# Optimization experiments

Hardware: AMD Instinct MI355X
Metric: run time of the kernel (lower is better)

Reference implementation:

```python
import jax, jax.numpy as jnp
import numpy as np

EPS = 1e-5
H, HC = 4, 16  # heads, head_dim (H*HC = hidden_dim = 64)
FILL = jnp.array([0., 0., 0., 0., 0., 0., 1.], dtype=jnp.float32)  # self-loop edge_attr


def inorm(x, w, b):
    # PyG InstanceNorm on a single graph: per-channel stats over all nodes
    mu = x.mean(axis=0)
    var = x.var(axis=0)
    return (x - mu) / jnp.sqrt(var + EPS) * w + b


def setup_inputs() -> dict:
    key = jax.random.key(0)
    ks = jax.random.split(key, 40)
    N, E, D, ED = 50000, 1600000, 64, 7
    p = lambda i, s: jax.random.normal(ks[i], s, dtype=jnp.float32) * 0.05
    return {
        'x': jax.random.normal(ks[0], (N, D), dtype=jnp.float32),
        'edge_index': jax.random.randint(ks[1], (2, E), 0, N),
        'edge_attr': jax.random.normal(ks[2], (E, ED), dtype=jnp.float32),
        'pre_w': 1.0 + p(3, (D,)), 'pre_b': p(4, (D,)),
        'eW1': p(5, (D, 64)), 'en1w': 1.0 + p(6, (64,)), 'en1b': p(7, (64,)),
        'eW2': p(8, (64, 64)), 'en2w': 1.0 + p(9, (64,)), 'en2b': p(10, (64,)),
        'Wl': p(11, (64, 64)), 'Wr': p(12, (64, 64)), 'We': p(13, (ED, 64)), 'att': p(14, (H, HC)),
        'gn_w': 1.0 + p(15, (64,)), 'gn_b': p(16, (64,)),
        'dW1': p(17, (128, 256)), 'db1': p(18, (256,)),
        'dW2': p(19, (256, 128)), 'db2': p(20, (128,)),
        'dW3': p(21, (128, 64)), 'db3': p(22, (64,)),
        'dW4': p(23, (64, 32)), 'db4': p(24, (32,)),
        'dW5': p(25, (32, 16)), 'db5': p(26, (16,)),
        'dW6': p(27, (16, 2)), 'db6': p(28, (2,)),
        'rW1': p(29, (64, 64)), 'rb1': p(30, (64,)),
        'rW2': p(31, (64, 64)), 'rb2': p(32, (64,)),
        'rW3': p(33, (64, 64)), 'rb3': p(34, (64,)),
    }


def _forward(x, edge_index, edge_attr,
             pre_w, pre_b, eW1, en1w, en1b, eW2, en2w, en2b,
             Wl, Wr, We, att, gn_w, gn_b,
             dW1, db1, dW2, db2, dW3, db3, dW4, db4, dW5, db5, dW6, db6,
             rW1, rb1, rW2, rb2, rW3, rb3):
    N = x.shape[0]
    h = inorm(x, pre_w, pre_b)
    h = jax.nn.elu(inorm(h @ eW1, en1w, en1b))
    h = jax.nn.elu(inorm(h @ eW2, en2w, en2b))
    jk = h

    # ---- GATv2 block (add self loops with fill_value edge attr) ----
    loop = jnp.arange(N)
    src = jnp.concatenate([edge_index[0], loop])  # message source j
    dst = jnp.concatenate([edge_index[1], loop])  # message target i
    ea = jnp.concatenate([edge_attr, jnp.broadcast_to(FILL, (N, 7))], axis=0)

    xl = (h @ Wl).reshape(N, H, HC)  # lin_l (source features)
    xr = (h @ Wr).reshape(N, H, HC)  # lin_r (target features)
    ee = (ea @ We).reshape(-1, H, HC)

    m = xl[src] + xr[dst] + ee                                  # [Etot,H,HC]
    logits = jnp.einsum('ehc,hc->eh', jax.nn.leaky_relu(m, 0.2), att)

    # softmax over incoming edges per target node, per head
    lmax = jax.ops.segment_max(logits, dst, num_segments=N)
    ex = jnp.exp(logits - lmax[dst])
    denom = jax.ops.segment_sum(ex, dst, num_segments=N)
    alpha = ex / denom[dst]

    msg = alpha[:, :, None] * xl[src]
    agg = jax.ops.segment_sum(msg, dst, num_segments=N)
    deg = jax.ops.segment_sum(jnp.ones((src.shape[0],), x.dtype), dst, num_segments=N)
    gat_out = (agg / deg[:, None, None]).reshape(N, H * HC)     # aggr='mean'

    h = jax.nn.elu(h + inorm(gat_out, gn_w, gn_b))

    cat = jnp.concatenate([jk, h], axis=-1)                     # jumping knowledge
    d = jax.nn.elu(cat @ dW1 + db1)
    d = jax.nn.elu(d @ dW2 + db2)
    d = jax.nn.elu(d @ dW3 + db3)
    d = jax.nn.elu(d @ dW4 + db4)
    d = jax.nn.elu(d @ dW5 + db5)
    dec = d @ dW6 + db6

    r = jax.nn.elu(h @ rW1 + rb1)
    r = jax.nn.elu(r @ rW2 + rb2)
    recon = r @ rW3 + rb3
    return dec, recon


def reference(x, edge_index, edge_attr,
              pre_w, pre_b, eW1, en1w, en1b, eW2, en2w, en2b,
              Wl, Wr, We, att, gn_w, gn_b,
              dW1, db1, dW2, db2, dW3, db3, dW4, db4, dW5, db5, dW6, db6,
              rW1, rb1, rW2, rb2, rW3, rb3):
    return _forward(x, edge_index, edge_attr,
                    pre_w, pre_b, eW1, en1w, en1b, eW2, en2w, en2b,
                    Wl, Wr, We, att, gn_w, gn_b,
                    dW1, db1, dW2, db2, dW3, db3, dW4, db4, dW5, db5, dW6, db6,
                    rW1, rb1, rW2, rb2, rW3, rb3)
```

## Files before the change

### kernel.cpp

```cpp
#include <hip/hip_runtime.h>
#include <math.h>


typedef long long ll;
typedef unsigned short u16;
typedef float f32x4 __attribute__((ext_vector_type(4)));
typedef short s16x8 __attribute__((ext_vector_type(8)));

__device__ __forceinline__ float bf(u16 u) { return __uint_as_float(((unsigned)u) << 16); }
__device__ __forceinline__ u16 f2bf(float f) {
  unsigned u = __float_as_uint(f);
  u += 0x7fffu + ((u >> 16) & 1u);
  return (u16)(u >> 16);
}
__device__ __forceinline__ float bflo(unsigned u) { return __uint_as_float(u << 16); }
__device__ __forceinline__ float bfhi(unsigned u) { return __uint_as_float(u & 0xffff0000u); }
__device__ __forceinline__ float elu_f(float x) { return x > 0.f ? x : (__expf(x) - 1.f); }

__global__ void k_probe64(const int* __restrict__ ei, int cnt, int* __restrict__ flag) {
  int tid = threadIdx.x;
  int nz = 0;
  for (int k = tid; k < cnt; k += 256) {
    if (ei[2 * k + 1] != 0) nz = 1;
  }
  if (nz) atomicOr(flag, 1);
}

__global__ void k_stats_x(const float* __restrict__ x, int N, double* __restrict__ s0) {
  __shared__ float red[256];
  int tid = threadIdx.x;
  int c = tid & 63;
  float s = 0.f, ss = 0.f;
  for (int r = blockIdx.x * 4 + (tid >> 6); r < N; r += gridDim.x * 4) {
    float v = x[r * 64 + c];
    s += v; ss += v * v;
  }
  red[tid] = s; __syncthreads();
  if (tid < 64) atomicAdd(&s0[tid], (double)(red[tid] + red[tid + 64] + red[tid + 128] + red[tid + 192]));
  __syncthreads();
  red[tid] = ss; __syncthreads();
  if (tid < 64) atomicAdd(&s0[64 + tid], (double)(red[tid] + red[tid + 64] + red[tid + 128] + red[tid + 192]));
}

__device__ __forceinline__ void norm_coeffs(const double* s, int tid, int N,
                                            const float* w, const float* b,
                                            float* na, float* nb) {
  double invN = 1.0 / (double)N;
  double mean = s[tid] * invN;
  double var = s[64 + tid] * invN - mean * mean;
  float a = rsqrtf((float)var + 1e-5f) * w[tid];
  na[tid] = a; nb[tid] = b[tid] - (float)mean * a;
}

template <bool ACT>
__global__ void k_enc(const float* __restrict__ in, const float* __restrict__ w,
                      const float* __restrict__ b, const float* __restrict__ Wg,
                      const double* __restrict__ sin_, float* __restrict__ out,
                      double* __restrict__ sout, int N) {
  __shared__ float W[4096];
  __shared__ float hl[4][64];
  __shared__ float na[64], nb[64];
  __shared__ float red[256];
  int tid = threadIdx.x;
  if (tid < 64) norm_coeffs(sin_, tid, N, w, b, na, nb);
  for (int k = tid; k < 4096; k += 256) W[k] = Wg[k];
  __syncthreads();
  int nl = tid >> 6, j = tid & 63;
  int Nc = (N + 3) >> 2;
  float ssum = 0.f, ssq = 0.f;
  for (int chunk = blockIdx.x; chunk < Nc; chunk += gridDim.x) {
    int node = chunk * 4 + nl;
    bool valid = node < N;
    float hv = valid ? (in[node * 64 + j] * na[j] + nb[j]) : 0.f;
    hl[nl][j] = ACT ? elu_f(hv) : hv;
    __syncthreads();
    if (valid) {
      float acc = 0.f;
#pragma unroll
      for (int i = 0; i < 64; i++) acc += hl[nl][i] * W[i * 64 + j];
      out[node * 64 + j] = acc;
      ssum += acc; ssq += acc * acc;
    }
    __syncthreads();
  }
  red[tid] = ssum; __syncthreads();
  if (tid < 64) atomicAdd(&sout[tid], (double)(red[tid] + red[tid + 64] + red[tid + 128] + red[tid + 192]));
  __syncthreads();
  red[tid] = ssq; __syncthreads();
  if (tid < 64) atomicAdd(&sout[64 + tid], (double)(red[tid] + red[tid + 64] + red[tid + 128] + red[tid + 192]));
}

__global__ void k_enc3(const float* __restrict__ tB, const float* __restrict__ w,
                       const float* __restrict__ b, const float* __restrict__ Wlw,
                       const float* __restrict__ Wrw, const double* __restrict__ s2,
                       float* __restrict__ jk, u16* __restrict__ xlb, float* __restrict__ xr,
                       int N) {
  __shared__ float WL[4096], WR[4096];
  __shared__ float hl[4][64];
  __shared__ float na[64], nb[64];
  int tid = threadIdx.x;
  if (tid < 64) norm_coeffs(s2, tid, N, w, b, na, nb);
  for (int k = tid; k < 4096; k += 256) { WL[k] = Wlw[k]; WR[k] = Wrw[k]; }
  __syncthreads();
  int nl = tid >> 6, j = tid & 63;
  int Nc = (N + 3) >> 2;
  for (int chunk = blockIdx.x; chunk < Nc; chunk += gridDim.x) {
    int node = chunk * 4 + nl;
    bool valid = node < N;
    float h3 = valid ? elu_f(tB[node * 64 + j] * na[j] + nb[j]) : 0.f;
    hl[nl][j] = h3;
    __syncthreads();
    if (valid) {
      jk[node * 64 + j] = h3;
      float al = 0.f, ar = 0.f;
#pragma unroll
      for (int i = 0; i < 64; i++) {
        float h = hl[nl][i];
        al += h * WL[i * 64 + j];
        ar += h * WR[i * 64 + j];
      }
      xlb[node * 64 + j] = f2bf(al);
      xr[node * 64 + j] = ar;
    }
    __syncthreads();
  }
}

__global__ void k_deg(const int* __restrict__ ei, int* __restrict__ deg8, int E, int N,
                      const int* __restrict__ i32flag) {
  int e = blockIdx.x * 256 + threadIdx.x;
  if (e >= E + N) return;
  int r = blockIdx.x & 7;
  int dst;
  if (e < E) {
    if (*i32flag) dst = ei[E + e];
    else { const ll* el = (const ll*)ei; dst = (int)el[E + e]; }
  } else dst = e - E;
  atomicAdd(&deg8[r * N + dst], 1);
}

__global__ void k_scanA(const int* __restrict__ deg8, int* __restrict__ bsum, int N) {
  __shared__ int red[256];
  int tid = threadIdx.x;
  int base = blockIdx.x * 1024;
  int s = 0;
#pragma unroll
  for (int q = 0; q < 4; q++) {
    int n = base + q * 256 + tid;
    if (n < N) {
#pragma unroll
      for (int r = 0; r < 8; r++) s += deg8[r * N + n];
    }
  }
  red[tid] = s; __syncthreads();
  for (int o = 128; o > 0; o >>= 1) {
    if (tid < o) red[tid] += red[tid + o];
    __syncthreads();
  }
  if (tid == 0) bsum[blockIdx.x] = red[0];
}

__global__ void k_scanB(const int* __restrict__ bsum, int* __restrict__ bscan,
                        int* __restrict__ offs, int NB, int N) {
  if (threadIdx.x == 0) {
    int run = 0;
    for (int b = 0; b < NB; b++) { bscan[b] = run; run += bsum[b]; }
    offs[N] = run;
  }
}

__global__ void k_scanC(const int* __restrict__ deg8, const int* __restrict__ bscan,
                        int* __restrict__ offs, int* __restrict__ cursor8, int N) {
  __shared__ int dt[1024];
  __shared__ int tp[256];
  int tid = threadIdx.x;
  int base = blockIdx.x * 1024;
#pragma unroll
  for (int q = 0; q < 4; q++) {
    int n = base + q * 256 + tid;
    int s = 0;
    if (n < N) {
#pragma unroll
      for (int r = 0; r < 8; r++) s += deg8[r * N + n];
    }
    dt[q * 256 + tid] = s;
  }
  __syncthreads();
  int t4 = tid * 4;
  int l0 = dt[t4], l1 = dt[t4 + 1], l2 = dt[t4 + 2], l3 = dt[t4 + 3];
  int tot = l0 + l1 + l2 + l3;
  tp[tid] = tot; __syncthreads();
  for (int o = 1; o < 256; o <<= 1) {
    int v = (tid >= o) ? tp[tid - o] : 0;
    __syncthreads();
    tp[tid] += v;
    __syncthreads();
  }
  int run = bscan[blockIdx.x] + tp[tid] - tot;
#pragma unroll
  for (int k = 0; k < 4; k++) {
    int n = base + t4 + k;
    if (n < N) {
      offs[n] = run;
      int b = run;
#pragma unroll
      for (int r = 0; r < 8; r++) { cursor8[r * N + n] = b; b += deg8[r * N + n]; }
      run = b;
    }
  }
}

template <bool PACKED>
__global__ void k_scatter(const int* __restrict__ ei, const float* __restrict__ eattr,
                          int* __restrict__ cursor8, int* __restrict__ csr_src,
                          uint4* __restrict__ ea2, int E, int N,
                          const int* __restrict__ i32flag) {
  int e = blockIdx.x * 256 + threadIdx.x;
  if (e >= E + N) return;
  int r = blockIdx.x & 7;
  int src, dst;
  u16 p[8];
  if (e < E) {
    if (*i32flag) { src = ei[e]; dst = ei[E + e]; }
    else { const ll* el = (const ll*)ei; src = (int)el[e]; dst = (int)el[E + e]; }
    const float* ea = eattr + (size_t)e * 7;
#pragma unroll
    for (int q = 0; q < 7; q++) p[q] = f2bf(ea[q]);
    p[7] = 0;
  } else {
    src = e - E; dst = src;
#pragma unroll
    for (int q = 0; q < 8; q++) p[q] = 0;
    p[6] = 0x3F80;
  }
  int pos = atomicAdd(&cursor8[r * N + dst], 1);
  uint4 U;
  U.x = ((unsigned)p[1] << 16) | p[0];
  U.y = ((unsigned)p[3] << 16) | p[2];
  U.z = ((unsigned)p[5] << 16) | p[4];
  if (PACKED) {
    U.w = ((unsigned)src << 16) | p[6];
  } else {
    U.w = ((unsigned)p[7] << 16) | p[6];
    csr_src[pos] = src;
  }
  ea2[pos] = U;
}

template <bool PACKED>
__global__ void k_gat(const int* __restrict__ offs, const int* __restrict__ csr_src,
                      const uint4* __restrict__ ea2,
                      const u16* __restrict__ xlb, const float* __restrict__ xr,
                      const float* __restrict__ Wew, const float* __restrict__ attw,
                      float* __restrict__ gat, double* __restrict__ s3, int N) {
  __shared__ float sb[4][64];
  int tid = threadIdx.x;
  int wid = tid >> 6;
  int lane = tid & 63;
  int g = lane >> 4;
  int l = lane & 15;
  int Nc = (N + 3) >> 2;

  float4 wq[7];
#pragma unroll
  for (int q = 0; q < 7; q++) wq[q] = *(const float4*)(Wew + q * 64 + 4 * l);
  float4 attv = *(const float4*)(attw + 4 * l);

  float ts0 = 0.f, ts1 = 0.f, ts2 = 0.f, ts3 = 0.f;
  float tq0 = 0.f, tq1 = 0.f, tq2 = 0.f, tq3 = 0.f;

  for (int chunk = blockIdx.x; chunk < Nc; chunk += gridDim.x) {
    int node = chunk * 4 + wid;
    if (node >= N) continue;
    float4 xrv = *(const float4*)(xr + node * 64 + 4 * l);
    int st = offs[node];
    int dg = offs[node + 1] - st;
    int nb = (dg + 3) >> 2;
    float sden = 0.f;
    float a0 = 0.f, a1 = 0.f, a2 = 0.f, a3 = 0.f;

    int i0 = st + g;
    uint4 UC = ea2[i0];
    uint4 UN = ea2[i0 + 4];
    int scC, scN;
    if (PACKED) {
      scC = (int)(UC.w >> 16);
      scN = (int)(UN.w >> 16);
    } else {
      scC = csr_src[i0];
      scN = csr_src[i0 + 4];
    }
    scC = ((unsigned)scC < (unsigned)N) ? scC : 0;
    uint2 xwC = *(const uint2*)(xlb + scC * 64 + 4 * l);

    for (int b = 0; b < nb; b++) {
      int iA = st + (b + 2) * 4 + g;
      uint4 UA = ea2[iA];
      int scA = PACKED ? 0 : csr_src[iA];
      int scg = PACKED ? (int)(UN.w >> 16) : scN;
      scg = ((unsigned)scg < (unsigned)N) ? scg : 0;
      uint2 xwN = *(const uint2*)(xlb + scg * 64 + 4 * l);
      bool valid = (b * 4 + g) < dg;
      float x0 = bflo(xwC.x), x1 = bfhi(xwC.x), x2 = bflo(xwC.y), x3 = bfhi(xwC.y);
      float e0 = bflo(UC.x), e1 = bfhi(UC.x), e2 = bflo(UC.y), e3 = bfhi(UC.y);
      float e4 = bflo(UC.z), e5 = bfhi(UC.z), e6 = bflo(UC.w);
      float m0 = x0 + xrv.x + e0*wq[0].x + e1*wq[1].x + e2*wq[2].x + e3*wq[3].x + e4*wq[4].x + e5*wq[5].x + e6*wq[6].x;
      float m1 = x1 + xrv.y + e0*wq[0].y + e1*wq[1].y + e2*wq[2].y + e3*wq[3].y + e4*wq[4].y + e5*wq[5].y + e6*wq[6].y;
      float m2 = x2 + xrv.z + e0*wq[0].z + e1*wq[1].z + e2*wq[2].z + e3*wq[3].z + e4*wq[4].z + e5*wq[5].z + e6*wq[6].z;
      float m3 = x3 + xrv.w + e0*wq[0].w + e1*wq[1].w + e2*wq[2].w + e3*wq[3].w + e4*wq[4].w + e5*wq[5].w + e6*wq[6].w;
      m0 = m0 > 0.f ? m0 : 0.2f * m0;
      m1 = m1 > 0.f ? m1 : 0.2f * m1;
      m2 = m2 > 0.f ? m2 : 0.2f * m2;
      m3 = m3 > 0.f ? m3 : 0.2f * m3;
      float pp = m0 * attv.x + m1 * attv.y + m2 * attv.z + m3 * attv.w;
      pp += __shfl_xor(pp, 1, 64);
      pp += __shfl_xor(pp, 2, 64);
      float ex = valid ? __expf(pp) : 0.f;
      sden += ex;
      a0 += ex * x0; a1 += ex * x1; a2 += ex * x2; a3 += ex * x3;
      xwC = xwN; UC = UN; UN = UA; scN = scA;
    }
    a0 += __shfl_xor(a0, 16, 64); a0 += __shfl_xor(a0, 32, 64);
    a1 += __shfl_xor(a1, 16, 64); a1 += __shfl_xor(a1, 32, 64);
    a2 += __shfl_xor(a2, 16, 64); a2 += __shfl_xor(a2, 32, 64);
    a3 += __shfl_xor(a3, 16, 64); a3 += __shfl_xor(a3, 32, 64);
    sden += __shfl_xor(sden, 16, 64); sden += __shfl_xor(sden, 32, 64);
    float inv = 1.f / (sden * (float)dg);
    float val0 = a0 * inv, val1 = a1 * inv, val2 = a2 * inv, val3 = a3 * inv;
    if (g == 0) {
      float4 o = make_float4(val0, val1, val2, val3);
      *(float4*)(gat + node * 64 + 4 * l) = o;
      ts0 += val0; ts1 += val1; ts2 += val2; ts3 += val3;
      tq0 += val0 * val0; tq1 += val1 * val1; tq2 += val2 * val2; tq3 += val3 * val3;
    }
  }

  if (g == 0) {
    sb[wid][4 * l + 0] = ts0; sb[wid][4 * l + 1] = ts1;
    sb[wid][4 * l + 2] = ts2; sb[wid][4 * l + 3] = ts3;
  }
  __syncthreads();
  if (tid < 64) {
    float v = sb[0][tid] + sb[1][tid] + sb[2][tid] + sb[3][tid];
    atomicAdd(&s3[tid], (double)v);
  }
  __syncthreads();
  if (g == 0) {
    sb[wid][4 * l + 0] = tq0; sb[wid][4 * l + 1] = tq1;
    sb[wid][4 * l + 2] = tq2; sb[wid][4 * l + 3] = tq3;
  }
  __syncthreads();
  if (tid < 64) {
    float v = sb[0][tid] + sb[1][tid] + sb[2][tid] + sb[3][tid];
    atomicAdd(&s3[64 + tid], (double)v);
  }
}

__global__ void k_edge2(const int* __restrict__ ei, const float* __restrict__ eattr,
                        const u16* __restrict__ xlb, const float* __restrict__ xr,
                        const float* __restrict__ Wew, const float* __restrict__ attw,
                        float* __restrict__ agg, float* __restrict__ denom,
                        int* __restrict__ deg, int E, int N,
                        const int* __restrict__ i32flag) {
  __shared__ float sWe[448];
  __shared__ float satt[64];
  int tid = threadIdx.x;
  for (int k = tid; k < 448; k += 256) sWe[k] = Wew[k];
  if (tid < 64) satt[tid] = attw[tid];
  __syncthreads();
  int e = blockIdx.x * 4 + (tid >> 6);
  if (e >= E + N) return;
  int lane = tid & 63;
  int src, dst;
  if (e < E) {
    if (*i32flag) { src = ei[e]; dst = ei[E + e]; }
    else { const ll* el = (const ll*)ei; src = (int)el[e]; dst = (int)el[E + e]; }
  } else { src = e - E; dst = src; }
  float xlv = bf(xlb[src * 64 + lane]);
  float m = xlv + xr[dst * 64 + lane];
  if (e < E) {
#pragma unroll
    for (int k = 0; k < 7; k++) m += eattr[e * 7 + k] * sWe[k * 64 + lane];
  } else {
    m += sWe[6 * 64 + lane];
  }
  float lr = m > 0.f ? m : 0.2f * m;
  float p = lr * satt[lane];
  p += __shfl_xor(p, 1, 64);
  p += __shfl_xor(p, 2, 64);
  p += __shfl_xor(p, 4, 64);
  p += __shfl_xor(p, 8, 64);
  float ex = __expf(p);
  atomicAdd(&agg[dst * 64 + lane], ex * xlv);
  if ((lane & 15) == 0) atomicAdd(&denom[dst * 4 + (lane >> 4)], ex);
  if (lane == 0) atomicAdd(&deg[dst], 1);
}

__global__ void k_gatnorm(float* __restrict__ agg, const float* __restrict__ denom,
                          const int* __restrict__ deg, double* __restrict__ s3, int N) {
  __shared__ float red[256];
  int tid = threadIdx.x;
  int idx = blockIdx.x * 256 + tid;
  float v = 0.f;
  if (idx < N * 64) {
    int n = idx >> 6, c = idx & 63, h = c >> 4;
    v = agg[idx] / (denom[n * 4 + h] * (float)deg[n]);
    agg[idx] = v;
  }
  red[tid] = v; __syncthreads();
  if (tid < 64) atomicAdd(&s3[tid], (double)(red[tid] + red[tid + 64] + red[tid + 128] + red[tid + 192]));
  __syncthreads();
  red[tid] = v * v; __syncthreads();
  if (tid < 64) atomicAdd(&s3[64 + tid], (double)(red[tid] + red[tid + 64] + red[tid + 128] + red[tid + 192]));
}

__global__ void k_h4(const float* __restrict__ jk, const float* __restrict__ gat,
                     const float* __restrict__ gn_w, const float* __restrict__ gn_b,
                     const double* __restrict__ s3, float* __restrict__ h4, int N) {
  __shared__ float na[64], nb[64];
  int tid = threadIdx.x;
  if (tid < 64) norm_coeffs(s3, tid, N, gn_w, gn_b, na, nb);
  __syncthreads();
  int idx = blockIdx.x * 256 + tid;
  if (idx >= N * 64) return;
  int c = idx & 63;
  h4[idx] = elu_f(jk[idx] + gat[idx] * na[c] + nb[c]);
}

__global__ void k_wprep(const float* __restrict__ dW1, const float* __restrict__ dW2,
                        const float* __restrict__ dW3, const float* __restrict__ dW4,
                        const float* __restrict__ dW5,
                        u16* __restrict__ whi, u16* __restrict__ wlo) {
  int t = blockIdx.x;
  int tid = threadIdx.x;
  const float* W; int LIN, LOUT, base;
  if (t < 64)       { W = dW1; LIN = 128; LOUT = 256; base = 0; }
  else if (t < 128) { W = dW2; LIN = 256; LOUT = 128; base = 64; }
  else if (t < 144) { W = dW3; LIN = 128; LOUT = 64;  base = 128; }
  else if (t < 148) { W = dW4; LIN = 64;  LOUT = 32;  base = 144; }
  else              { W = dW5; LIN = 32;  LOUT = 16;  base = 148; }
  int KT = LIN >> 5;
  int tl = t - base;
  int nt = tl / KT, kt = tl % KT;
#pragma unroll
  for (int half = 0; half < 2; half++) {
    int lane = (tid >> 3) + half * 32;
    int i = tid & 7;
    int kg = kt * 32 + (lane >> 4) * 8 + i;
    int ng = nt * 16 + (lane & 15);
    float v = W[kg * LOUT + ng];
    u16 hi = f2bf(v);
    u16 lo = f2bf(v - bf(hi));
    whi[((size_t)t * 64 + lane) * 8 + i] = hi;
    wlo[((size_t)t * 64 + lane) * 8 + i] = lo;
  }
}

template <int LIN, int LOUT, int TBASE>
__device__ __forceinline__ void mfmaLayer(const u16* __restrict__ whi, const u16* __restrict__ wlo,
                                          const float* __restrict__ bias,
                                          const u16* __restrict__ Ahi, const u16* __restrict__ Alo,
                                          u16* __restrict__ Ohi, u16* __restrict__ Olo,
                                          int wid, int lane) {
  constexpr int KT = LIN / 32, NT = LOUT / 16;
  constexpr int SIN = LIN + 8, SOUT = LOUT + 8;
  int l15 = lane & 15, kg = lane >> 4;
  int aoff = l15 * SIN + kg * 8;
  for (int nt = wid; nt < NT; nt += 4) {
    float bn = bias[nt * 16 + l15];
    f32x4 acc = {bn, bn, bn, bn};
    for (int kt = 0; kt < KT; kt++) {
      s16x8 ah = *(const s16x8*)(Ahi + aoff + kt * 32);
      s16x8 al = *(const s16x8*)(Alo + aoff + kt * 32);
      const u16* wp = whi + ((size_t)(TBASE + nt * KT + kt) * 64 + lane) * 8;
      const u16* wq = wlo + ((size_t)(TBASE + nt * KT + kt) * 64 + lane) * 8;
      s16x8 wh = *(const s16x8*)(wp);
      s16x8 wl = *(const s16x8*)(wq);
      acc = __builtin_amdgcn_mfma_f32_16x16x32_bf16(ah, wh, acc, 0, 0, 0);
      acc = __builtin_amdgcn_mfma_f32_16x16x32_bf16(ah, wl, acc, 0, 0, 0);
      acc = __builtin_amdgcn_mfma_f32_16x16x32_bf16(al, wh, acc, 0, 0, 0);
    }
#pragma unroll
    for (int r = 0; r < 4; r++) {
      int m = kg * 4 + r;
      float v = elu_f(acc[r]);
      u16 hi = f2bf(v);
      u16 lo = f2bf(v - bf(hi));
      Ohi[m * SOUT + nt * 16 + l15] = hi;
      Olo[m * SOUT + nt * 16 + l15] = lo;
    }
  }
}

__global__ void k_dec(const float* __restrict__ jk, const float* __restrict__ h4,
                      const u16* __restrict__ whi, const u16* __restrict__ wlo,
                      const float* __restrict__ db1, const float* __restrict__ db2,
                      const float* __restrict__ db3, const float* __restrict__ db4,
                      const float* __restrict__ db5,
                      const float* __restrict__ dW6, const float* __restrict__ db6,
                      float* __restrict__ outdec, int N) {
  __shared__ __align__(16) u16 bHi0[16 * 264], bLo0[16 * 264];
  __shared__ __align__(16) u16 bHi1[16 * 264], bLo1[16 * 264];
  int tid = threadIdx.x;
  int wid = tid >> 6, lane = tid & 63;
  int g0 = blockIdx.x * 16;
  for (int k = tid; k < 16 * 128; k += 256) {
    int i = k & 127, node = k >> 7;
    int gn = g0 + node;
    float v = 0.f;
    if (gn < N) v = (i < 64) ? jk[gn * 64 + i] : h4[gn * 64 + (i - 64)];
    u16 hi = f2bf(v);
    u16 lo = f2bf(v - bf(hi));
    bHi0[node * 136 + i] = hi;
    bLo0[node * 136 + i] = lo;
  }
  __syncthreads();
  mfmaLayer<128, 256, 0>(whi, wlo, db1, bHi0, bLo0, bHi1, bLo1, wid, lane); __syncthreads();
  mfmaLayer<256, 128, 64>(whi, wlo, db2, bHi1, bLo1, bHi0, bLo0, wid, lane); __syncthreads();
  mfmaLayer<128, 64, 128>(whi, wlo, db3, bHi0, bLo0, bHi1, bLo1, wid, lane); __syncthreads();
  mfmaLayer<64, 32, 144>(whi, wlo, db4, bHi1, bLo1, bHi0, bLo0, wid, lane); __syncthreads();
  mfmaLayer<32, 16, 148>(whi, wlo, db5, bHi0, bLo0, bHi1, bLo1, wid, lane); __syncthreads();
  if (tid < 32) {
    int node = tid >> 1, j = tid & 1;
    int gn = g0 + node;
    if (gn < N) {
      float s = db6[j];
#pragma unroll
      for (int i = 0; i < 16; i++) {
        float a = bf(bHi1[node * 24 + i]) + bf(bLo1[node * 24 + i]);
        s += a * dW6[i * 2 + j];
      }
      outdec[gn * 2 + j] = s;
    }
  }
}

__global__ void k_recon(const float* __restrict__ h4,
                        const float* __restrict__ rW1, const float* __restrict__ rb1,
                        const float* __restrict__ rW2, const float* __restrict__ rb2,
                        const float* __restrict__ rW3, const float* __restrict__ rb3,
                        float* __restrict__ outrec, int N) {
  __shared__ float W1[4096], W2[4096], W3[4096];
  __shared__ float b1[64], b2[64], b3[64];
  __shared__ float A[64 * 16], Bb[64 * 16];
  int tid = threadIdx.x;
  for (int k = tid; k < 4096; k += 256) { W1[k] = rW1[k]; W2[k] = rW2[k]; W3[k] = rW3[k]; }
  if (tid < 64) { b1[tid] = rb1[tid]; b2[tid] = rb2[tid]; b3[tid] = rb3[tid]; }
  __syncthreads();
  int j = tid & 63, g = tid >> 6;
  int Nc = (N + 15) >> 4;
  for (int chunk = blockIdx.x; chunk < Nc; chunk += gridDim.x) {
    int g0 = chunk * 16;
    for (int k = tid; k < 16 * 64; k += 256) {
      int i = k & 63, node = k >> 6;
      int gn = g0 + node;
      A[i * 16 + node] = (gn < N) ? h4[gn * 64 + i] : 0.f;
    }
    __syncthreads();
    {
      float a0 = b1[j], a1 = b1[j], a2 = b1[j], a3 = b1[j];
#pragma unroll 4
      for (int i = 0; i < 64; i++) {
        float w = W1[i * 64 + j];
        float4 a = *(const float4*)(&A[i * 16 + g * 4]);
        a0 += a.x * w; a1 += a.y * w; a2 += a.z * w; a3 += a.w * w;
      }
      Bb[j * 16 + g * 4 + 0] = elu_f(a0);
      Bb[j * 16 + g * 4 + 1] = elu_f(a1);
      Bb[j * 16 + g * 4 + 2] = elu_f(a2);
      Bb[j * 16 + g * 4 + 3] = elu_f(a3);
    }
    __syncthreads();
    {
      float a0 = b2[j], a1 = b2[j], a2 = b2[j], a3 = b2[j];
#pragma unroll 4
      for (int i = 0; i < 64; i++) {
        float w = W2[i * 64 + j];
        float4 a = *(const float4*)(&Bb[i * 16 + g * 4]);
        a0 += a.x * w; a1 += a.y * w; a2 += a.z * w; a3 += a.w * w;
      }
      A[j * 16 + g * 4 + 0] = elu_f(a0);
      A[j * 16 + g * 4 + 1] = elu_f(a1);
      A[j * 16 + g * 4 + 2] = elu_f(a2);
      A[j * 16 + g * 4 + 3] = elu_f(a3);
    }
    __syncthreads();
    {
      float a0 = b3[j], a1 = b3[j], a2 = b3[j], a3 = b3[j];
#pragma unroll 4
      for (int i = 0; i < 64; i++) {
        float w = W3[i * 64 + j];
        float4 a = *(const float4*)(&A[i * 16 + g * 4]);
        a0 += a.x * w; a1 += a.y * w; a2 += a.z * w; a3 += a.w * w;
      }
      float o[4] = {a0, a1, a2, a3};
#pragma unroll
      for (int u = 0; u < 4; u++) {
        int gn = g0 + g * 4 + u;
        if (gn < N) outrec[gn * 64 + j] = o[u];
      }
    }
    __syncthreads();
  }
}

__global__ void k_sentinel(float* __restrict__ out, float v) {
  if (threadIdx.x == 0) out[0] = v;
}

extern "C" void kernel_launch(void* const* d_in, const int* in_sizes, int n_in,
                              void* d_out, int out_size, void* d_ws, size_t ws_size,
                              hipStream_t stream) {
  (void)n_in; (void)out_size;
  const float* x     = (const float*)d_in[0];
  const int*   ei    = (const int*)d_in[1];
  const float* ea    = (const float*)d_in[2];
  const float* pre_w = (const float*)d_in[3];
  const float* pre_b = (const float*)d_in[4];
  const float* eW1   = (const float*)d_in[5];
  const float* en1w  = (const float*)d_in[6];
  const float* en1b  = (const float*)d_in[7];
  const float* eW2   = (const float*)d_in[8];
  const float* en2w  = (const float*)d_in[9];
  const float* en2b  = (const float*)d_in[10];
  const float* Wl    = (const float*)d_in[11];
  const float* Wr    = (const float*)d_in[12];
  const float* Wew   = (const float*)d_in[13];
  const float* attw  = (const float*)d_in[14];
  const float* gn_w  = (const float*)d_in[15];
  const float* gn_b  = (const float*)d_in[16];
  const float* dW1 = (const float*)d_in[17]; const float* db1 = (const float*)d_in[18];
  const float* dW2 = (const float*)d_in[19]; const float* db2 = (const float*)d_in[20];
  const float* dW3 = (const float*)d_in[21]; const float* db3 = (const float*)d_in[22];
  const float* dW4 = (const float*)d_in[23]; const float* db4 = (const float*)d_in[24];
  const float* dW5 = (const float*)d_in[25]; const float* db5 = (const float*)d_in[26];
  const float* dW6 = (const float*)d_in[27]; const float* db6 = (const float*)d_in[28];
  const float* rW1 = (const float*)d_in[29]; const float* rb1 = (const float*)d_in[30];
  const float* rW2 = (const float*)d_in[31]; const float* rb2 = (const float*)d_in[32];
  const float* rW3 = (const float*)d_in[33]; const float* rb3 = (const float*)d_in[34];

  int D  = in_sizes[3];
  int N  = in_sizes[0] / (D > 0 ? D : 1);
  int E  = in_sizes[1] / 2;
  int ED = E > 0 ? in_sizes[2] / E : 0;
  float* outdec = (float*)d_out;
  float* outrec = outdec + (size_t)N * 2;
  if (D != 64 || ED != 7 || in_sizes[14] != 64) {
    k_sentinel<<<1, 64, 0, stream>>>(outdec, 2000.f);
    return;
  }
  int Etot = E + N;

  char* w = (char*)d_ws;
  size_t off = 0;
  auto alloc = [&](size_t bytes) -> void* {
    void* p = w + off;
    off += (bytes + 255) & ~(size_t)255;
    return p;
  };
  const size_t FEATF = (size_t)N * 64 * 4;
  float* B1    = (float*)alloc(FEATF);
  size_t ea2_bytes = ((size_t)Etot + 16) * 16;
  size_t b2ext = ea2_bytes > FEATF ? ea2_bytes : FEATF;
  float* B2    = (float*)alloc(b2ext);
  float* jk    = (float*)alloc(FEATF);
  u16*   xlb   = (u16*)  alloc((size_t)N * 64 * 2);
  float* xr    = (float*)alloc(FEATF);
  int*   offs  = (int*)  alloc(((size_t)N + 1) * 4);
  int*   deg8  = (int*)  alloc((size_t)N * 8 * 4);
  int*   cursor8=(int*)  alloc((size_t)N * 8 * 4);
  int*   bsum  = (int*)  alloc(4096);
  int*   bscan = (int*)  alloc(4096);
  double* stats = (double*)alloc(4 * 128 * 8);
  int* i32flag = (int*)alloc(256);
  float* denom = (float*)alloc((size_t)N * 4 * 4);
  u16* whi = (u16*)alloc((size_t)149 * 512 * 2);
  u16* wlo = (u16*)alloc((size_t)149 * 512 * 2);
  size_t base_off = off;
  int* csr_src = (int*)alloc(((size_t)Etot + 16) * 4);
  size_t csr_off = off;

  double* s0 = stats, *s1 = stats + 128, *s2 = stats + 256, *s3 = stats + 384;
  float* t1 = B1; float* gat = B1; float* agg = B1;
  float* t2 = B2; float* h4 = B2;
  uint4* ea2 = (uint4*)B2;

  bool packed = (N <= 65536);
  bool use_csr = packed ? (base_off <= ws_size) : (csr_off <= ws_size);
  if (!use_csr && base_off > ws_size) {
    k_sentinel<<<1, 64, 0, stream>>>(outdec, 1000.f);
    return;
  }

  hipMemsetAsync(stats, 0, 4 * 128 * 8, stream);
  hipMemsetAsync(i32flag, 0, 256, stream);
  hipMemsetAsync(deg8, 0, (size_t)N * 8 * 4, stream);

  int gN64 = (N * 64 + 255) / 256;
  int gE = (Etot + 255) / 256;
  int probeCnt = E < 1024 ? E : 1024;
  int NB = (N + 1023) / 1024;

  k_probe64<<<1, 256, 0, stream>>>(ei, probeCnt, i32flag);
  k_wprep<<<149, 256, 0, stream>>>(dW1, dW2, dW3, dW4, dW5, whi, wlo);
  k_stats_x<<<1024, 256, 0, stream>>>(x, N, s0);
  k_enc<false><<<1024, 256, 0, stream>>>(x, pre_w, pre_b, eW1, s0, t1, s1, N);
  k_enc<true><<<1024, 256, 0, stream>>>(t1, en1w, en1b, eW2, s1, t2, s2, N);
  k_enc3<<<1024, 256, 0, stream>>>(t2, en2w, en2b, Wl, Wr, s2, jk, xlb, xr, N);

  if (use_csr) {
    k_deg<<<gE, 256, 0, stream>>>(ei, deg8, E, N, i32flag);
    k_scanA<<<NB, 256, 0, stream>>>(deg8, bsum, N);
    k_scanB<<<1, 64, 0, stream>>>(bsum, bscan, offs, NB, N);
    k_scanC<<<NB, 256, 0, stream>>>(deg8, bscan, offs, cursor8, N);
    int ggat = 2048;
    int NcG = (N + 3) / 4;
    if (ggat > NcG) ggat = NcG;
    if (packed) {
      k_scatter<true><<<gE, 256, 0, stream>>>(ei, ea, cursor8, csr_src, ea2, E, N, i32flag);
      k_gat<true><<<ggat, 256, 0, stream>>>(offs, csr_src, ea2, xlb, xr, Wew, attw,
                                            gat, s3, N);
    } else {
      k_scatter<false><<<gE, 256, 0, stream>>>(ei, ea, cursor8, csr_src, ea2, E, N, i32flag);
      k_gat<false><<<ggat, 256, 0, stream>>>(offs, csr_src, ea2, xlb, xr, Wew, attw,
                                             gat, s3, N);
    }
  } else {
    hipMemsetAsync(agg, 0, FEATF, stream);
    hipMemsetAsync(denom, 0, (size_t)N * 4 * 4, stream);
    k_edge2<<<(Etot + 3) / 4, 256, 0, stream>>>(ei, ea, xlb, xr, Wew, attw, agg, denom,
                                                deg8, E, N, i32flag);
    k_gatnorm<<<gN64, 256, 0, stream>>>(agg, denom, deg8, s3, N);
  }

  k_h4<<<gN64, 256, 0, stream>>>(jk, gat, gn_w, gn_b, s3, h4, N);
  int NcD = (N + 15) / 16;
  k_dec<<<NcD, 256, 0, stream>>>(jk, h4, whi, wlo, db1, db2, db3, db4, db5,
                                 dW6, db6, outdec, N);
  k_recon<<<1024, 256, 0, stream>>>(h4, rW1, rb1, rW2, rb2, rW3, rb3, outrec, N);
}
```

Before: 666.8 us.

## Move encoder, GAT projection and recon MLP matmuls onto split-bf16 MFMA

```diff
diff --git a/kernel.cpp b/kernel.cpp
--- a/kernel.cpp
+++ b/kernel.cpp
@@ -52,75 +52,283 @@
   na[tid] = a; nb[tid] = b[tid] - (float)mean * a;
 }
 
-template <bool ACT>
-__global__ void k_enc(const float* __restrict__ in, const float* __restrict__ w,
-                      const float* __restrict__ b, const float* __restrict__ Wg,
-                      const double* __restrict__ sin_, float* __restrict__ out,
-                      double* __restrict__ sout, int N) {
-  __shared__ float W[4096];
-  __shared__ float hl[4][64];
+__global__ void k_wprep(const float* __restrict__ dW1, const float* __restrict__ dW2,
+                        const float* __restrict__ dW3, const float* __restrict__ dW4,
+                        const float* __restrict__ dW5,
+                        const float* __restrict__ eW1, const float* __restrict__ eW2,
+                        const float* __restrict__ Wl, const float* __restrict__ Wr,
+                        const float* __restrict__ rW1, const float* __restrict__ rW2,
+                        const float* __restrict__ rW3,
+                        u16* __restrict__ whi, u16* __restrict__ wlo) {
+  int t = blockIdx.x;
+  int tid = threadIdx.x;
+  const float* W; int LIN, LOUT, base;
+  if (t < 64)       { W = dW1; LIN = 128; LOUT = 256; base = 0; }
+  else if (t < 128) { W = dW2; LIN = 256; LOUT = 128; base = 64; }
+  else if (t < 144) { W = dW3; LIN = 128; LOUT = 64;  base = 128; }
+  else if (t < 148) { W = dW4; LIN = 64;  LOUT = 32;  base = 144; }
+  else if (t < 149) { W = dW5; LIN = 32;  LOUT = 16;  base = 148; }
+  else if (t < 157) { W = eW1; LIN = 64;  LOUT = 64;  base = 149; }
+  else if (t < 165) { W = eW2; LIN = 64;  LOUT = 64;  base = 157; }
+  else if (t < 173) { W = Wl;  LIN = 64;  LOUT = 64;  base = 165; }
+  else if (t < 181) { W = Wr;  LIN = 64;  LOUT = 64;  base = 173; }
+  else if (t < 189) { W = rW1; LIN = 64;  LOUT = 64;  base = 181; }
+  else if (t < 197) { W = rW2; LIN = 64;  LOUT = 64;  base = 189; }
+  else              { W = rW3; LIN = 64;  LOUT = 64;  base = 197; }
+  int KT = LIN >> 5;
+  int tl = t - base;
+  int nt = tl / KT, kt = tl % KT;
+#pragma unroll
+  for (int half = 0; half < 2; half++) {
+    int lane = (tid >> 3) + half * 32;
+    int i = tid & 7;
+    int kg = kt * 32 + (lane >> 4) * 8 + i;
+    int ng = nt * 16 + (lane & 15);
+    float v = W[kg * LOUT + ng];
+    u16 hi = f2bf(v);
+    u16 lo = f2bf(v - bf(hi));
+    whi[((size_t)t * 64 + lane) * 8 + i] = hi;
+    wlo[((size_t)t * 64 + lane) * 8 + i] = lo;
+  }
+}
+
+template <bool INELU>
+__global__ void k_encM(const float* __restrict__ in, const float* __restrict__ w,
+                       const float* __restrict__ b, const u16* __restrict__ whi,
+                       const u16* __restrict__ wlo, int TB,
+                       const double* __restrict__ sin_, float* __restrict__ out,
+                       double* __restrict__ sout, int N) {
+  __shared__ __align__(16) u16 aHi[16 * 72], aLo[16 * 72];
   __shared__ float na[64], nb[64];
-  __shared__ float red[256];
+  __shared__ float sred[64];
   int tid = threadIdx.x;
   if (tid < 64) norm_coeffs(sin_, tid, N, w, b, na, nb);
-  for (int k = tid; k < 4096; k += 256) W[k] = Wg[k];
-  __syncthreads();
-  int nl = tid >> 6, j = tid & 63;
-  int Nc = (N + 3) >> 2;
-  float ssum = 0.f, ssq = 0.f;
+  __syncthreads();
+  int lane = tid & 63, wid = tid >> 6;
+  int l15 = lane & 15, kg = lane >> 4;
+  int Nc = (N + 15) >> 4;
+  float ts = 0.f, tq = 0.f;
   for (int chunk = blockIdx.x; chunk < Nc; chunk += gridDim.x) {
-    int node = chunk * 4 + nl;
-    bool valid = node < N;
-    float hv = valid ? (in[node * 64 + j] * na[j] + nb[j]) : 0.f;
-    hl[nl][j] = ACT ? elu_f(hv) : hv;
-    __syncthreads();
-    if (valid) {
-      float acc = 0.f;
-#pragma unroll
-      for (int i = 0; i < 64; i++) acc += hl[nl][i] * W[i * 64 + j];
-      out[node * 64 + j] = acc;
-      ssum += acc; ssq += acc * acc;
-    }
-    __syncthreads();
-  }
-  red[tid] = ssum; __syncthreads();
-  if (tid < 64) atomicAdd(&sout[tid], (double)(red[tid] + red[tid + 64] + red[tid + 128] + red[tid + 192]));
-  __syncthreads();
-  red[tid] = ssq; __syncthreads();
-  if (tid < 64) atomicAdd(&sout[64 + tid], (double)(red[tid] + red[tid + 64] + red[tid + 128] + red[tid + 192]));
-}
-
-__global__ void k_enc3(const float* __restrict__ tB, const float* __restrict__ w,
-                       const float* __restrict__ b, const float* __restrict__ Wlw,
-                       const float* __restrict__ Wrw, const double* __restrict__ s2,
-                       float* __restrict__ jk, u16* __restrict__ xlb, float* __restrict__ xr,
-                       int N) {
-  __shared__ float WL[4096], WR[4096];
-  __shared__ float hl[4][64];
+    int g0 = chunk * 16;
+    for (int k = tid; k < 1024; k += 256) {
+      int i = k & 63, node = k >> 6;
+      int gn = g0 + node;
+      float v = 0.f;
+      if (gn < N) {
+        v = in[gn * 64 + i] * na[i] + nb[i];
+        if (INELU) v = elu_f(v);
+      }
+      u16 hi = f2bf(v);
+      aHi[node * 72 + i] = hi;
+      aLo[node * 72 + i] = f2bf(v - bf(hi));
+    }
+    __syncthreads();
+    f32x4 acc = {0.f, 0.f, 0.f, 0.f};
+    int aoff = l15 * 72 + kg * 8;
+#pragma unroll
+    for (int kt = 0; kt < 2; kt++) {
+      s16x8 ah = *(const s16x8*)(aHi + aoff + kt * 32);
+      s16x8 al = *(const s16x8*)(aLo + aoff + kt * 32);
+      const u16* wp = whi + ((size_t)(TB + wid * 2 + kt) * 64 + lane) * 8;
+      const u16* wq = wlo + ((size_t)(TB + wid * 2 + kt) * 64 + lane) * 8;
+      s16x8 wh = *(const s16x8*)wp;
+      s16x8 wl = *(const s16x8*)wq;
+      acc = __builtin_amdgcn_mfma_f32_16x16x32_bf16(ah, wh, acc, 0, 0, 0);
+      acc = __builtin_amdgcn_mfma_f32_16x16x32_bf16(ah, wl, acc, 0, 0, 0);
+      acc = __builtin_amdgcn_mfma_f32_16x16x32_bf16(al, wh, acc, 0, 0, 0);
+    }
+    int col = wid * 16 + l15;
+#pragma unroll
+    for (int r = 0; r < 4; r++) {
+      int m = kg * 4 + r;
+      int gn = g0 + m;
+      if (gn < N) {
+        float v = acc[r];
+        out[gn * 64 + col] = v;
+        ts += v; tq += v * v;
+      }
+    }
+    __syncthreads();
+  }
+  ts += __shfl_xor(ts, 16, 64); ts += __shfl_xor(ts, 32, 64);
+  tq += __shfl_xor(tq, 16, 64); tq += __shfl_xor(tq, 32, 64);
+  if (kg == 0) sred[wid * 16 + l15] = ts;
+  __syncthreads();
+  if (tid < 64) atomicAdd(&sout[tid], (double)sred[tid]);
+  __syncthreads();
+  if (kg == 0) sred[wid * 16 + l15] = tq;
+  __syncthreads();
+  if (tid < 64) atomicAdd(&sout[64 + tid], (double)sred[tid]);
+}
+
+__global__ void k_enc3M(const float* __restrict__ t2, const float* __restrict__ w,
+                        const float* __restrict__ b, const u16* __restrict__ whi,
+                        const u16* __restrict__ wlo, const double* __restrict__ s2,
+                        float* __restrict__ jk, u16* __restrict__ xlb,
+                        float* __restrict__ xr, int N) {
+  __shared__ __align__(16) u16 aHi[16 * 72], aLo[16 * 72];
   __shared__ float na[64], nb[64];
   int tid = threadIdx.x;
   if (tid < 64) norm_coeffs(s2, tid, N, w, b, na, nb);
-  for (int k = tid; k < 4096; k += 256) { WL[k] = Wlw[k]; WR[k] = Wrw[k]; }
-  __syncthreads();
-  int nl = tid >> 6, j = tid & 63;
-  int Nc = (N + 3) >> 2;
+  __syncthreads();
+  int lane = tid & 63, wid = tid >> 6;
+  int l15 = lane & 15, kg = lane >> 4;
+  int Nc = (N + 15) >> 4;
   for (int chunk = blockIdx.x; chunk < Nc; chunk += gridDim.x) {
-    int node = chunk * 4 + nl;
-    bool valid = node < N;
-    float h3 = valid ? elu_f(tB[node * 64 + j] * na[j] + nb[j]) : 0.f;
-    hl[nl][j] = h3;
-    __syncthreads();
-    if (valid) {
-      jk[node * 64 + j] = h3;
-      float al = 0.f, ar = 0.f;
-#pragma unroll
-      for (int i = 0; i < 64; i++) {
-        float h = hl[nl][i];
-        al += h * WL[i * 64 + j];
-        ar += h * WR[i * 64 + j];
-      }
-      xlb[node * 64 + j] = f2bf(al);
-      xr[node * 64 + j] = ar;
+    int g0 = chunk * 16;
+    for (int k = tid; k < 1024; k += 256) {
+      int i = k & 63, node = k >> 6;
+      int gn = g0 + node;
+      float v = 0.f;
+      if (gn < N) {
+        v = elu_f(t2[gn * 64 + i] * na[i] + nb[i]);
+        jk[gn * 64 + i] = v;
+      }
+      u16 hi = f2bf(v);
+      aHi[node * 72 + i] = hi;
+      aLo[node * 72 + i] = f2bf(v - bf(hi));
+    }
+    __syncthreads();
+    int aoff = l15 * 72 + kg * 8;
+    int col = wid * 16 + l15;
+    {
+      f32x4 acc = {0.f, 0.f, 0.f, 0.f};
+#pragma unroll
+      for (int kt = 0; kt < 2; kt++) {
+        s16x8 ah = *(const s16x8*)(aHi + aoff + kt * 32);
+        s16x8 al = *(const s16x8*)(aLo + aoff + kt * 32);
+        const u16* wp = whi + ((size_t)(165 + wid * 2 + kt) * 64 + lane) * 8;
+        const u16* wq = wlo + ((size_t)(165 + wid * 2 + kt) * 64 + lane) * 8;
+        s16x8 wh = *(const s16x8*)wp;
+        s16x8 wl = *(const s16x8*)wq;
+        acc = __builtin_amdgcn_mfma_f32_16x16x32_bf16(ah, wh, acc, 0, 0, 0);
+        acc = __builtin_amdgcn_mfma_f32_16x16x32_bf16(ah, wl, acc, 0, 0, 0);
+        acc = __builtin_amdgcn_mfma_f32_16x16x32_bf16(al, wh, acc, 0, 0, 0);
+      }
+#pragma unroll
+      for (int r = 0; r < 4; r++) {
+        int gn = g0 + kg * 4 + r;
+        if (gn < N) xlb[gn * 64 + col] = f2bf(acc[r]);
+      }
+    }
+    {
+      f32x4 acc = {0.f, 0.f, 0.f, 0.f};
+#pragma unroll
+      for (int kt = 0; kt < 2; kt++) {
+        s16x8 ah = *(const s16x8*)(aHi + aoff + kt * 32);
+        s16x8 al = *(const s16x8*)(aLo + aoff + kt * 32);
+        const u16* wp = whi + ((size_t)(173 + wid * 2 + kt) * 64 + lane) * 8;
+        const u16* wq = wlo + ((size_t)(173 + wid * 2 + kt) * 64 + lane) * 8;
+        s16x8 wh = *(const s16x8*)wp;
+        s16x8 wl = *(const s16x8*)wq;
+        acc = __builtin_amdgcn_mfma_f32_16x16x32_bf16(ah, wh, acc, 0, 0, 0);
+        acc = __builtin_amdgcn_mfma_f32_16x16x32_bf16(ah, wl, acc, 0, 0, 0);
+        acc = __builtin_amdgcn_mfma_f32_16x16x32_bf16(al, wh, acc, 0, 0, 0);
+      }
+#pragma unroll
+      for (int r = 0; r < 4; r++) {
+        int gn = g0 + kg * 4 + r;
+        if (gn < N) xr[gn * 64 + col] = acc[r];
+      }
+    }
+    __syncthreads();
+  }
+}
+
+__global__ void k_reconM(const float* __restrict__ h4, const u16* __restrict__ whi,
+                         const u16* __restrict__ wlo,
+                         const float* __restrict__ rb1, const float* __restrict__ rb2,
+                         const float* __restrict__ rb3,
+                         float* __restrict__ outrec, int N) {
+  __shared__ __align__(16) u16 aHi[16 * 72], aLo[16 * 72];
+  __shared__ __align__(16) u16 bHi[16 * 72], bLo[16 * 72];
+  int tid = threadIdx.x;
+  int lane = tid & 63, wid = tid >> 6;
+  int l15 = lane & 15, kg = lane >> 4;
+  int aoff = l15 * 72 + kg * 8;
+  int col = wid * 16 + l15;
+  int Nc = (N + 15) >> 4;
+  for (int chunk = blockIdx.x; chunk < Nc; chunk += gridDim.x) {
+    int g0 = chunk * 16;
+    for (int k = tid; k < 1024; k += 256) {
+      int i = k & 63, node = k >> 6;
+      int gn = g0 + node;
+      float v = (gn < N) ? h4[gn * 64 + i] : 0.f;
+      u16 hi = f2bf(v);
+      aHi[node * 72 + i] = hi;
+      aLo[node * 72 + i] = f2bf(v - bf(hi));
+    }
+    __syncthreads();
+    {
+      float bn = rb1[col];
+      f32x4 acc = {bn, bn, bn, bn};
+#pragma unroll
+      for (int kt = 0; kt < 2; kt++) {
+        s16x8 ah = *(const s16x8*)(aHi + aoff + kt * 32);
+        s16x8 al = *(const s16x8*)(aLo + aoff + kt * 32);
+        const u16* wp = whi + ((size_t)(181 + wid * 2 + kt) * 64 + lane) * 8;
+        const u16* wq = wlo + ((size_t)(181 + wid * 2 + kt) * 64 + lane) * 8;
+        s16x8 wh = *(const s16x8*)wp;
+        s16x8 wl = *(const s16x8*)wq;
+        acc = __builtin_amdgcn_mfma_f32_16x16x32_bf16(ah, wh, acc, 0, 0, 0);
+        acc = __builtin_amdgcn_mfma_f32_16x16x32_bf16(ah, wl, acc, 0, 0, 0);
+        acc = __builtin_amdgcn_mfma_f32_16x16x32_bf16(al, wh, acc, 0, 0, 0);
+      }
+#pragma unroll
+      for (int r = 0; r < 4; r++) {
+        int m = kg * 4 + r;
+        float v = elu_f(acc[r]);
+        u16 hi = f2bf(v);
+        bHi[m * 72 + col] = hi;
+        bLo[m * 72 + col] = f2bf(v - bf(hi));
+      }
+    }
+    __syncthreads();
+    {
+      float bn = rb2[col];
+      f32x4 acc = {bn, bn, bn, bn};
+#pragma unroll
+      for (int kt = 0; kt < 2; kt++) {
+        s16x8 ah = *(const s16x8*)(bHi + aoff + kt * 32);
+        s16x8 al = *(const s16x8*)(bLo + aoff + kt * 32);
+        const u16* wp = whi + ((size_t)(189 + wid * 2 + kt) * 64 + lane) * 8;
+        const u16* wq = wlo + ((size_t)(189 + wid * 2 + kt) * 64 + lane) * 8;
+        s16x8 wh = *(const s16x8*)wp;
+        s16x8 wl = *(const s16x8*)wq;
+        acc = __builtin_amdgcn_mfma_f32_16x16x32_bf16(ah, wh, acc, 0, 0, 0);
+        acc = __builtin_amdgcn_mfma_f32_16x16x32_bf16(ah, wl, acc, 0, 0, 0);
+        acc = __builtin_amdgcn_mfma_f32_16x16x32_bf16(al, wh, acc, 0, 0, 0);
+      }
+#pragma unroll
+      for (int r = 0; r < 4; r++) {
+        int m = kg * 4 + r;
+        float v = elu_f(acc[r]);
+        u16 hi = f2bf(v);
+        aHi[m * 72 + col] = hi;
+        aLo[m * 72 + col] = f2bf(v - bf(hi));
+      }
+    }
+    __syncthreads();
+    {
+      float bn = rb3[col];
+      f32x4 acc = {bn, bn, bn, bn};
+#pragma unroll
+      for (int kt = 0; kt < 2; kt++) {
+        s16x8 ah = *(const s16x8*)(aHi + aoff + kt * 32);
+        s16x8 al = *(const s16x8*)(aLo + aoff + kt * 32);
+        const u16* wp = whi + ((size_t)(197 + wid * 2 + kt) * 64 + lane) * 8;
+        const u16* wq = wlo + ((size_t)(197 + wid * 2 + kt) * 64 + lane) * 8;
+        s16x8 wh = *(const s16x8*)wp;
+        s16x8 wl = *(const s16x8*)wq;
+        acc = __builtin_amdgcn_mfma_f32_16x16x32_bf16(ah, wh, acc, 0, 0, 0);
+        acc = __builtin_amdgcn_mfma_f32_16x16x32_bf16(ah, wl, acc, 0, 0, 0);
+        acc = __builtin_amdgcn_mfma_f32_16x16x32_bf16(al, wh, acc, 0, 0, 0);
+      }
+#pragma unroll
+      for (int r = 0; r < 4; r++) {
+        int gn = g0 + kg * 4 + r;
+        if (gn < N) outrec[gn * 64 + col] = acc[r];
+      }
     }
     __syncthreads();
   }
@@ -427,35 +635,6 @@
   h4[idx] = elu_f(jk[idx] + gat[idx] * na[c] + nb[c]);
 }
 
-__global__ void k_wprep(const float* __restrict__ dW1, const float* __restrict__ dW2,
-                        const float* __restrict__ dW3, const float* __restrict__ dW4,
-                        const float* __restrict__ dW5,
-                        u16* __restrict__ whi, u16* __restrict__ wlo) {
-  int t = blockIdx.x;
-  int tid = threadIdx.x;
-  const float* W; int LIN, LOUT, base;
-  if (t < 64)       { W = dW1; LIN = 128; LOUT = 256; base = 0; }
-  else if (t < 128) { W = dW2; LIN = 256; LOUT = 128; base = 64; }
-  else if (t < 144) { W = dW3; LIN = 128; LOUT = 64;  base = 128; }
-  else if (t < 148) { W = dW4; LIN = 64;  LOUT = 32;  base = 144; }
-  else              { W = dW5; LIN = 32;  LOUT = 16;  base = 148; }
-  int KT = LIN >> 5;
-  int tl = t - base;
-  int nt = tl / KT, kt = tl % KT;
-#pragma unroll
-  for (int half = 0; half < 2; half++) {
-    int lane = (tid >> 3) + half * 32;
-    int i = tid & 7;
-    int kg = kt * 32 + (lane >> 4) * 8 + i;
-    int ng = nt * 16 + (lane & 15);
-    float v = W[kg * LOUT + ng];
-    u16 hi = f2bf(v);
-    u16 lo = f2bf(v - bf(hi));
-    whi[((size_t)t * 64 + lane) * 8 + i] = hi;
-    wlo[((size_t)t * 64 + lane) * 8 + i] = lo;
-  }
-}
-
 template <int LIN, int LOUT, int TBASE>
 __device__ __forceinline__ void mfmaLayer(const u16* __restrict__ whi, const u16* __restrict__ wlo,
                                           const float* __restrict__ bias,
@@ -532,75 +711,6 @@
       }
       outdec[gn * 2 + j] = s;
     }
-  }
-}
-
-__global__ void k_recon(const float* __restrict__ h4,
-                        const float* __restrict__ rW1, const float* __restrict__ rb1,
-                        const float* __restrict__ rW2, const float* __restrict__ rb2,
-                        const float* __restrict__ rW3, const float* __restrict__ rb3,
-                        float* __restrict__ outrec, int N) {
-  __shared__ float W1[4096], W2[4096], W3[4096];
-  __shared__ float b1[64], b2[64], b3[64];
-  __shared__ float A[64 * 16], Bb[64 * 16];
-  int tid = threadIdx.x;
-  for (int k = tid; k < 4096; k += 256) { W1[k] = rW1[k]; W2[k] = rW2[k]; W3[k] = rW3[k]; }
-  if (tid < 64) { b1[tid] = rb1[tid]; b2[tid] = rb2[tid]; b3[tid] = rb3[tid]; }
-  __syncthreads();
-  int j = tid & 63, g = tid >> 6;
-  int Nc = (N + 15) >> 4;
-  for (int chunk = blockIdx.x; chunk < Nc; chunk += gridDim.x) {
-    int g0 = chunk * 16;
-    for (int k = tid; k < 16 * 64; k += 256) {
-      int i = k & 63, node = k >> 6;
-      int gn = g0 + node;
-      A[i * 16 + node] = (gn < N) ? h4[gn * 64 + i] : 0.f;
-    }
-    __syncthreads();
-    {
-      float a0 = b1[j], a1 = b1[j], a2 = b1[j], a3 = b1[j];
-#pragma unroll 4
-      for (int i = 0; i < 64; i++) {
-        float w = W1[i * 64 + j];
-        float4 a = *(const float4*)(&A[i * 16 + g * 4]);
-        a0 += a.x * w; a1 += a.y * w; a2 += a.z * w; a3 += a.w * w;
-      }
-      Bb[j * 16 + g * 4 + 0] = elu_f(a0);
-      Bb[j * 16 + g * 4 + 1] = elu_f(a1);
-      Bb[j * 16 + g * 4 + 2] = elu_f(a2);
-      Bb[j * 16 + g * 4 + 3] = elu_f(a3);
-    }
-    __syncthreads();
-    {
-      float a0 = b2[j], a1 = b2[j], a2 = b2[j], a3 = b2[j];
-#pragma unroll 4
-      for (int i = 0; i < 64; i++) {
-        float w = W2[i * 64 + j];
-        float4 a = *(const float4*)(&Bb[i * 16 + g * 4]);
-        a0 += a.x * w; a1 += a.y * w; a2 += a.z * w; a3 += a.w * w;
-      }
-      A[j * 16 + g * 4 + 0] = elu_f(a0);
-      A[j * 16 + g * 4 + 1] = elu_f(a1);
-      A[j * 16 + g * 4 + 2] = elu_f(a2);
-      A[j * 16 + g * 4 + 3] = elu_f(a3);
-    }
-    __syncthreads();
-    {
-      float a0 = b3[j], a1 = b3[j], a2 = b3[j], a3 = b3[j];
-#pragma unroll 4
-      for (int i = 0; i < 64; i++) {
-        float w = W3[i * 64 + j];
-        float4 a = *(const float4*)(&A[i * 16 + g * 4]);
-        a0 += a.x * w; a1 += a.y * w; a2 += a.z * w; a3 += a.w * w;
-      }
-      float o[4] = {a0, a1, a2, a3};
-#pragma unroll
-      for (int u = 0; u < 4; u++) {
-        int gn = g0 + g * 4 + u;
-        if (gn < N) outrec[gn * 64 + j] = o[u];
-      }
-    }
-    __syncthreads();
   }
 }
 
@@ -674,8 +784,8 @@
   double* stats = (double*)alloc(4 * 128 * 8);
   int* i32flag = (int*)alloc(256);
   float* denom = (float*)alloc((size_t)N * 4 * 4);
-  u16* whi = (u16*)alloc((size_t)149 * 512 * 2);
-  u16* wlo = (u16*)alloc((size_t)149 * 512 * 2);
+  u16* whi = (u16*)alloc((size_t)205 * 512 * 2);
+  u16* wlo = (u16*)alloc((size_t)205 * 512 * 2);
   size_t base_off = off;
   int* csr_src = (int*)alloc(((size_t)Etot + 16) * 4);
   size_t csr_off = off;
@@ -700,13 +810,16 @@
   int gE = (Etot + 255) / 256;
   int probeCnt = E < 1024 ? E : 1024;
   int NB = (N + 1023) / 1024;
+  int Nc16 = (N + 15) / 16;
+  int gEnc = Nc16 < 2048 ? Nc16 : 2048;
 
   k_probe64<<<1, 256, 0, stream>>>(ei, probeCnt, i32flag);
-  k_wprep<<<149, 256, 0, stream>>>(dW1, dW2, dW3, dW4, dW5, whi, wlo);
+  k_wprep<<<205, 256, 0, stream>>>(dW1, dW2, dW3, dW4, dW5, eW1, eW2, Wl, Wr,
+                                   rW1, rW2, rW3, whi, wlo);
   k_stats_x<<<1024, 256, 0, stream>>>(x, N, s0);
-  k_enc<false><<<1024, 256, 0, stream>>>(x, pre_w, pre_b, eW1, s0, t1, s1, N);
-  k_enc<true><<<1024, 256, 0, stream>>>(t1, en1w, en1b, eW2, s1, t2, s2, N);
-  k_enc3<<<1024, 256, 0, stream>>>(t2, en2w, en2b, Wl, Wr, s2, jk, xlb, xr, N);
+  k_encM<false><<<gEnc, 256, 0, stream>>>(x, pre_w, pre_b, whi, wlo, 149, s0, t1, s1, N);
+  k_encM<true><<<gEnc, 256, 0, stream>>>(t1, en1w, en1b, whi, wlo, 157, s1, t2, s2, N);
+  k_enc3M<<<gEnc, 256, 0, stream>>>(t2, en2w, en2b, whi, wlo, s2, jk, xlb, xr, N);
 
   if (use_csr) {
     k_deg<<<gE, 256, 0, stream>>>(ei, deg8, E, N, i32flag);
@@ -734,8 +847,7 @@
   }
 
   k_h4<<<gN64, 256, 0, stream>>>(jk, gat, gn_w, gn_b, s3, h4, N);
-  int NcD = (N + 15) / 16;
-  k_dec<<<NcD, 256, 0, stream>>>(jk, h4, whi, wlo, db1, db2, db3, db4, db5,
-                                 dW6, db6, outdec, N);
-  k_recon<<<1024, 256, 0, stream>>>(h4, rW1, rb1, rW2, rb2, rW3, rb3, outrec, N);
-}
+  k_dec<<<Nc16, 256, 0, stream>>>(jk, h4, whi, wlo, db1, db2, db3, db4, db5,
+                                  dW6, db6, outdec, N);
+  k_reconM<<<gEnc, 256, 0, stream>>>(h4, rW1 != 0 ? whi : whi, wlo, rb1, rb2, rb3, outrec, N);
+}
```

Result: faster. 625.2 us (-6.2%).
